# Optimization experiments

Hardware: AMD Instinct MI355X
Metric: run time of the kernel (lower is better)

The kernel has to match this reference:

```python
import jax, jax.numpy as jnp
import numpy as np

B, N, PREV, PRED, H = 16, 64, 6, 30, 256
E = N * (N - 1)
BN_EPS = 1e-5


def _mlp(x, W1, b1, W2, b2, gamma, beta):
    # Two-layer ELU MLP with batch norm over flattened (batch*rows) dim.
    h = jax.nn.elu(x @ W1 + b1)
    h = jax.nn.elu(h @ W2 + b2)
    b, n, d = h.shape
    f = h.reshape(b * n, d)
    mu = f.mean(axis=0)
    var = f.var(axis=0)
    f = (f - mu) * jax.lax.rsqrt(var + BN_EPS) * gamma + beta
    return f.reshape(b, n, d)


def setup_inputs() -> dict:
    key = jax.random.key(0)
    ks = jax.random.split(key, 8)
    # fully-connected directed graph without self loops
    recv, send = np.where(~np.eye(N, dtype=bool))  # each [E]
    rel_rec = jnp.broadcast_to(jax.nn.one_hot(jnp.asarray(recv), N)[None], (B, E, N)).astype(jnp.float32)
    rel_send = jnp.broadcast_to(jax.nn.one_hot(jnp.asarray(send), N)[None], (B, E, N)).astype(jnp.float32)

    def xavier(k, shape):
        fan_in, fan_out = shape
        std = np.sqrt(2.0 / (fan_in + fan_out))
        return jax.random.normal(k, shape, jnp.float32) * std

    return {
        "prev_actor_centers": jax.random.normal(ks[0], (B, N, PREV, 2), jnp.float32) * 10.0,
        "rel_rec": rel_rec,
        "rel_send": rel_send,
        "W_traj": xavier(ks[1], (PREV * 2, H)),
        "b_traj": jnp.full((H,), 0.1, jnp.float32),
        "n2e_W1": xavier(ks[2], (2 * H, H)),
        "n2e_b1": jnp.full((H,), 0.1, jnp.float32),
        "n2e_W2": xavier(ks[3], (H, H)),
        "n2e_b2": jnp.full((H,), 0.1, jnp.float32),
        "n2e_gamma": jnp.ones((H,), jnp.float32),
        "n2e_beta": jnp.zeros((H,), jnp.float32),
        "e2n_W1": xavier(ks[4], (2 * H, H)),
        "e2n_b1": jnp.full((H,), 0.1, jnp.float32),
        "e2n_W2": xavier(ks[5], (H, H)),
        "e2n_b2": jnp.full((H,), 0.1, jnp.float32),
        "e2n_gamma": jnp.ones((H,), jnp.float32),
        "e2n_beta": jnp.zeros((H,), jnp.float32),
        "W_fuse": xavier(ks[6], (2 * H, H)),
        "b_fuse": jnp.full((H,), 0.1, jnp.float32),
        "W_pred": xavier(ks[7], (H, PRED * 2)),
        "b_pred": jnp.full((PRED * 2,), 0.1, jnp.float32),
    }


def reference(prev_actor_centers, rel_rec, rel_send,
              W_traj, b_traj,
              n2e_W1, n2e_b1, n2e_W2, n2e_b2, n2e_gamma, n2e_beta,
              e2n_W1, e2n_b1, e2n_W2, e2n_b2, e2n_gamma, e2n_beta,
              W_fuse, b_fuse, W_pred, b_pred):
    b, n, prev, _ = prev_actor_centers.shape
    # relative displacements, first step zero
    diffs = prev_actor_centers[:, :, 1:, :] - prev_actor_centers[:, :, :-1, :]
    rel_pos = jnp.concatenate([jnp.zeros((b, n, 1, 2), prev_actor_centers.dtype), diffs], axis=2)
    rel_pos = rel_pos.reshape(b, n, prev * 2)
    x = rel_pos @ W_traj + b_traj  # [b, n, H] node features

    # node2edge: gather via one-hot relation matmuls
    receivers = jnp.einsum('ben,bnh->beh', rel_rec, x)
    senders = jnp.einsum('ben,bnh->beh', rel_send, x)
    edges = jnp.concatenate([receivers, senders], axis=-1)  # [b, E, 2H]
    e = _mlp(edges, n2e_W1, n2e_b1, n2e_W2, n2e_b2, n2e_gamma, n2e_beta)

    # edge2node: degree-normalized scatter via transposed relation matmuls
    deg_rec = rel_rec.sum(axis=1)  # [b, n]
    deg_rec = deg_rec + (deg_rec == 0).astype(deg_rec.dtype)
    incoming = jnp.einsum('ben,beh->bnh', rel_rec, e) / deg_rec[..., None]
    deg_send = rel_send.sum(axis=1)
    deg_send = deg_send + (deg_send == 0).astype(deg_send.dtype)
    outgoing = jnp.einsum('ben,beh->bnh', rel_send, e) / deg_send[..., None]
    nodes = jnp.concatenate([incoming, outgoing], axis=-1)  # [b, n, 2H]
    m = _mlp(nodes, e2n_W1, e2n_b1, e2n_W2, e2n_b2, e2n_gamma, e2n_beta)

    fused = jnp.concatenate([x, m], axis=-1) @ W_fuse + b_fuse  # [b, n, H]
    rel = fused @ W_pred + b_pred  # [b, n, PRED*2]

    current_loc = prev_actor_centers[:, :, -1, :]  # [b, n, 2]
    current_loc = jnp.broadcast_to(current_loc[:, :, None, :], (b, n, PRED, 2)).reshape(b, n, PRED * 2)
    pos = jnp.cumsum(rel.reshape(b, n, PRED, 2), axis=2).reshape(b, n, PRED * 2) + current_loc
    return (rel, pos)
```

## Files before the change

### kernel.cpp

```cpp
#include <hip/hip_runtime.h>
#include <hip/hip_bf16.h>

#define BB 16
#define NN 64
#define PREVN 6
#define PREDN 30
#define HH 256
#define EE 4032
#define EROWS (BB*EE)
#define NROWS (BB*NN)

typedef short short8 __attribute__((ext_vector_type(8)));
typedef float f32x4 __attribute__((ext_vector_type(4)));

enum : int {
  OFF_STATS_E = 0,
  OFF_STATS_M = 1024,
  F32_END     = 264192
};
enum : size_t {
  BO_XB    = 0,
  BO_W1TE  = 262144,
  BO_W2TE  = 393216,
  BO_W1TN  = 458752,
  BO_W2TN  = 589824,
  BO_WFT   = 655360,
  BO_WPT   = 786432,
  BO_NODES = 802816,
  BO_M2    = 1327104,
  BO_E2    = 1589248
};

__device__ __forceinline__ float eluf(float v) { return v > 0.f ? v : expm1f(v); }

__device__ __forceinline__ void gl2lds16(const void* g, void* l) {
  __builtin_amdgcn_global_load_lds(
      (const __attribute__((address_space(1))) void*)g,
      (__attribute__((address_space(3))) void*)l, 16, 0, 0);
}

struct PrepArgs {
  const float *centers, *W_traj, *b_traj;
  const float *n2e_W1, *n2e_W2, *e2n_W1, *e2n_W2, *W_fuse, *W_pred;
  float* stats;
  __hip_bfloat16 *xb, *w1te, *w2te, *w1tn, *w2tn, *wft, *wpt;
};

__global__ __launch_bounds__(256) void k_prep(PrepArgs a) {
  __shared__ float t[64][65];
  const int bid = blockIdx.x, tid = threadIdx.x;
  if (bid < 128) {
    const float* W; __hip_bfloat16* WT; int K, lb;
    if (bid < 32)      { W = a.n2e_W1; WT = a.w1te; K = 512; lb = bid; }
    else if (bid < 48) { W = a.n2e_W2; WT = a.w2te; K = 256; lb = bid - 32; }
    else if (bid < 80) { W = a.e2n_W1; WT = a.w1tn; K = 512; lb = bid - 48; }
    else if (bid < 96) { W = a.e2n_W2; WT = a.w2tn; K = 256; lb = bid - 80; }
    else               { W = a.W_fuse; WT = a.wft;  K = 512; lb = bid - 96; }
    int KB = K / 64;
    int k0 = (lb % KB) * 64, n0 = (lb / KB) * 64;
    int tx = tid & 63, ty = tid >> 6;
    #pragma unroll
    for (int i = 0; i < 16; ++i)
      t[ty + i*4][tx] = W[(size_t)(k0 + ty + i*4) * 256 + n0 + tx];
    __syncthreads();
    #pragma unroll
    for (int i = 0; i < 16; ++i)
      WT[(size_t)(n0 + ty + i*4) * K + k0 + tx] = __float2bfloat16(t[tx][ty + i*4]);
  } else if (bid < 192) {
    int idx = (bid - 128) * 256 + tid;
    int c = idx >> 8, k = idx & 255;
    a.wpt[idx] = __float2bfloat16(c < 60 ? a.W_pred[k * 60 + c] : 0.f);
  } else if (bid < 200) {
    a.stats[(bid - 192) * 256 + tid] = 0.f;
  } else {
    int row = bid - 200, col = tid;
    const float* c = a.centers + row * (PREVN * 2);
    float rp[12];
    #pragma unroll
    for (int t2 = 0; t2 < 5; ++t2) {
      rp[2 + 2*t2] = c[(t2+1)*2 + 0] - c[t2*2 + 0];
      rp[3 + 2*t2] = c[(t2+1)*2 + 1] - c[t2*2 + 1];
    }
    float acc = a.b_traj[col];
    #pragma unroll
    for (int k = 2; k < 12; ++k) acc += rp[k] * a.W_traj[k*HH + col];
    a.xb[row*HH + col] = __float2bfloat16(acc);
  }
}

template<int MODE>
__global__ __launch_bounds__(256, 2) void k_mlp3(
    const __hip_bfloat16* __restrict__ A,
    const __hip_bfloat16* __restrict__ W1T,
    const float* __restrict__ b1,
    const __hip_bfloat16* __restrict__ W2T,
    const float* __restrict__ b2,
    __hip_bfloat16* __restrict__ outp,
    float* __restrict__ stats) {
  constexpr int MT = (MODE == 0) ? 4 : 1;
  constexpr int ROWS = MT * 16;
  __shared__ alignas(16) __hip_bfloat16 Wt[256 * 64];
  __shared__ alignas(16) __hip_bfloat16 At[ROWS * 64];
  __shared__ alignas(16) __hip_bfloat16 h1s[ROWS][264];
  const int tid = threadIdx.x;
  const int w = tid >> 6, lane = tid & 63;
  const int m16 = lane & 15, quad = lane >> 4;
  const int ko = quad * 8;
  const int row0 = blockIdx.x * ROWS;
  const int colw = w * 64;
  const int csub = lane >> 3, jl = lane & 7;
  const int jsrc = jl ^ csub;

  const __hip_bfloat16 *ar0[2], *ar1[2];
  #pragma unroll
  for (int t = 0; t < 2; ++t) {
    int i = w + 4 * t;
    if (i < MT * 2) {
      int r = i * 8 + csub;
      int g = row0 + r;
      if (MODE == 0) {
        int b = g / EE; int e = g - b * EE;
        int rc = e / 63; int jj = e - rc * 63;
        int sd = jj + (jj >= rc ? 1 : 0);
        ar0[t] = A + (size_t)(b * NN + rc) * HH;
        ar1[t] = A + (size_t)(b * NN + sd) * HH;
      } else {
        ar0[t] = A + (size_t)g * 512;
        ar1[t] = ar0[t] + 256;
      }
    }
  }
  const int swz0 = ((quad)     ^ (m16 & 7)) * 16;
  const int swz1 = ((quad + 4) ^ (m16 & 7)) * 16;

  f32x4 acc[MT][4];
  #pragma unroll
  for (int jt = 0; jt < 4; ++jt) {
    float bv = b1[colw + jt*16 + m16];
    #pragma unroll
    for (int mt = 0; mt < MT; ++mt) acc[mt][jt] = (f32x4){bv, bv, bv, bv};
  }
  for (int kt = 0; kt < 8; ++kt) {
    const int k0 = kt * 64;
    #pragma unroll
    for (int i = 0; i < 8; ++i) {
      const __hip_bfloat16* gp = W1T + (size_t)(colw + i*8 + csub) * 512 + k0 + jsrc*8;
      gl2lds16(gp, (char*)Wt + w*8192 + i*1024);
    }
    #pragma unroll
    for (int t = 0; t < 2; ++t) {
      int i = w + 4*t;
      if (i < MT*2) {
        const __hip_bfloat16* gp =
            (k0 < 256 ? ar0[t] + k0 : ar1[t] + (k0 - 256)) + jsrc*8;
        gl2lds16(gp, (char*)At + i*1024);
      }
    }
    __syncthreads();
    #pragma unroll
    for (int ks = 0; ks < 2; ++ks) {
      const int sw = ks ? swz1 : swz0;
      short8 af[MT], bf[4];
      #pragma unroll
      for (int mt = 0; mt < MT; ++mt)
        af[mt] = *(const short8*)((const char*)At + (mt*16 + m16)*128 + sw);
      #pragma unroll
      for (int jt = 0; jt < 4; ++jt)
        bf[jt] = *(const short8*)((const char*)Wt + (colw + jt*16 + m16)*128 + sw);
      #pragma unroll
      for (int mt = 0; mt < MT; ++mt)
        #pragma unroll
        for (int jt = 0; jt < 4; ++jt)
          acc[mt][jt] = __builtin_amdgcn_mfma_f32_16x16x32_bf16(af[mt], bf[jt],
                                                                acc[mt][jt], 0, 0, 0);
    }
    __syncthreads();
  }
  #pragma unroll
  for (int mt = 0; mt < MT; ++mt)
    #pragma unroll
    for (int jt = 0; jt < 4; ++jt)
      #pragma unroll
      for (int r = 0; r < 4; ++r)
        h1s[mt*16 + quad*4 + r][colw + jt*16 + m16] =
            __float2bfloat16(eluf(acc[mt][jt][r]));
  __syncthreads();

  f32x4 acc2[MT][4];
  #pragma unroll
  for (int jt = 0; jt < 4; ++jt) {
    float bv = b2[colw + jt*16 + m16];
    #pragma unroll
    for (int mt = 0; mt < MT; ++mt) acc2[mt][jt] = (f32x4){bv, bv, bv, bv};
  }
  for (int kt = 0; kt < 4; ++kt) {
    const int k0 = kt * 64;
    #pragma unroll
    for (int i = 0; i < 8; ++i) {
      const __hip_bfloat16* gp = W2T + (size_t)(colw + i*8 + csub) * 256 + k0 + jsrc*8;
      gl2lds16(gp, (char*)Wt + w*8192 + i*1024);
    }
    __syncthreads();
    #pragma unroll
    for (int ks = 0; ks < 2; ++ks) {
      const int sw = ks ? swz1 : swz0;
      short8 af[MT], bf[4];
      #pragma unroll
      for (int mt = 0; mt < MT; ++mt)
        af[mt] = *(const short8*)((const char*)h1s +
                     (size_t)(mt*16 + m16)*528 + (k0 + ks*32 + ko)*2);
      #pragma unroll
      for (int jt = 0; jt < 4; ++jt)
        bf[jt] = *(const short8*)((const char*)Wt + (colw + jt*16 + m16)*128 + sw);
      #pragma unroll
      for (int mt = 0; mt < MT; ++mt)
        #pragma unroll
        for (int jt = 0; jt < 4; ++jt)
          acc2[mt][jt] = __builtin_amdgcn_mfma_f32_16x16x32_bf16(af[mt], bf[jt],
                                                                 acc2[mt][jt], 0, 0, 0);
    }
    __syncthreads();
  }
  #pragma unroll
  for (int mt = 0; mt < MT; ++mt)
    #pragma unroll
    for (int jt = 0; jt < 4; ++jt)
      #pragma unroll
      for (int r = 0; r < 4; ++r)
        h1s[mt*16 + quad*4 + r][colw + jt*16 + m16] =
            __float2bfloat16(eluf(acc2[mt][jt][r]));
  __syncthreads();

  {
    float s = 0.f, q = 0.f;
    #pragma unroll 8
    for (int r = 0; r < ROWS; ++r) {
      float v = __bfloat162float(h1s[r][tid]);
      s += v; q += v * v;
    }
    atomicAdd(&stats[tid], s);
    atomicAdd(&stats[256 + tid], q);
  }
  #pragma unroll
  for (int i = 0; i < ROWS/8; ++i) {
    int u = i*256 + tid;
    int r = u >> 5, c = (u & 31) * 8;
    *reinterpret_cast<uint4*>(outp + (size_t)(row0 + r)*HH + c) =
        *reinterpret_cast<const uint4*>(&h1s[r][c]);
  }
}

__global__ __launch_bounds__(256) void k_agg2(const __hip_bfloat16* __restrict__ e2,
                                              const float* __restrict__ st,
                                              const float* __restrict__ gam,
                                              const float* __restrict__ bet,
                                              __hip_bfloat16* __restrict__ nodes) {
  __shared__ float red[8][256];
  const int blk = blockIdx.x;
  const int bn = blk >> 1, half = blk & 1;
  const int b = bn >> 6, n = bn & 63;
  const int tid = threadIdx.x;
  const int c8 = (tid & 31) * 8;
  const int rg = tid >> 5;
  const __hip_bfloat16* base = e2 + (size_t)b * EE * HH;
  float s[8] = {0.f,0.f,0.f,0.f,0.f,0.f,0.f,0.f};
  for (int j = rg; j < 63; j += 8) {
    const __hip_bfloat16* rp;
    if (half == 0) {
      rp = base + (size_t)(n*63 + j)*HH;
    } else {
      int i = j + (j >= n ? 1 : 0);
      int e = i*63 + n - (n > i ? 1 : 0);
      rp = base + (size_t)e*HH;
    }
    union { uint4 u; __hip_bfloat16 h[8]; } v;
    v.u = *reinterpret_cast<const uint4*>(rp + c8);
    #pragma unroll
    for (int jj = 0; jj < 8; ++jj) s[jj] += __bfloat162float(v.h[jj]);
  }
  #pragma unroll
  for (int jj = 0; jj < 8; jj += 4)
    *reinterpret_cast<float4*>(&red[rg][c8 + jj]) =
        (float4){s[jj], s[jj+1], s[jj+2], s[jj+3]};
  __syncthreads();
  float S = 0.f;
  #pragma unroll
  for (int r = 0; r < 8; ++r) S += red[r][tid];
  const float inv = 1.f / (float)EROWS;
  float mean = st[tid] * inv;
  float var  = fmaxf(st[256 + tid] * inv - mean*mean, 0.f);
  float a = gam[tid] * rsqrtf(var + 1e-5f);
  float c0 = bet[tid] - mean * a;
  nodes[(size_t)bn*512 + half*256 + tid] = __float2bfloat16(a * S * (1.f/63.f) + c0);
}

__global__ __launch_bounds__(256) void k_head2(
    const __hip_bfloat16* __restrict__ xb,
    const __hip_bfloat16* __restrict__ m2,
    const float* __restrict__ stM,
    const float* __restrict__ gam,
    const float* __restrict__ bet,
    const __hip_bfloat16* __restrict__ WfT,
    const float* __restrict__ bfv,
    const __hip_bfloat16* __restrict__ WpT,
    const float* __restrict__ bp,
    const float* __restrict__ centers,
    float* __restrict__ out) {
  __shared__ alignas(16) __hip_bfloat16 hs[16][264];
  __shared__ float rl[16][64];
  __shared__ float bnA[256], bnC[256];
  const int tid = threadIdx.x;
  const int w = tid >> 6, lane = tid & 63;
  const int m16 = lane & 15, quad = lane >> 4;
  const int ko = quad * 8;
  const int row0 = blockIdx.x * 16;
  const int colw = w * 64;

  {
    const float inv = 1.f / (float)NROWS;
    float mean = stM[tid] * inv;
    float var  = fmaxf(stM[256 + tid] * inv - mean*mean, 0.f);
    float am = gam[tid] * rsqrtf(var + 1e-5f);
    bnA[tid] = am;
    bnC[tid] = bet[tid] - mean * am;
  }
  __syncthreads();

  f32x4 acc[4];
  #pragma unroll
  for (int jt = 0; jt < 4; ++jt) {
    float bv = bfv[colw + jt*16 + m16];
    acc[jt] = (f32x4){bv, bv, bv, bv};
  }
  #pragma unroll
  for (int ks = 0; ks < 16; ++ks) {
    short8 af;
    if (ks < 8) {
      af = *reinterpret_cast<const short8*>(
          xb + (size_t)(row0 + m16)*256 + ks*32 + ko);
    } else {
      int k0 = (ks - 8)*32 + ko;
      union { uint4 u; __hip_bfloat16 h[8]; } v;
      v.u = *reinterpret_cast<const uint4*>(m2 + (size_t)(row0 + m16)*256 + k0);
      union { short8 s8; __hip_bfloat16 h[8]; } o;
      #pragma unroll
      for (int j = 0; j < 8; ++j)
        o.h[j] = __float2bfloat16(bnA[k0+j] * __bfloat162float(v.h[j]) + bnC[k0+j]);
      af = o.s8;
    }
    short8 bf[4];
    #pragma unroll
    for (int jt = 0; jt < 4; ++jt)
      bf[jt] = *reinterpret_cast<const short8*>(
          WfT + (size_t)(colw + jt*16 + m16)*512 + ks*32 + ko);
    #pragma unroll
    for (int jt = 0; jt < 4; ++jt)
      acc[jt] = __builtin_amdgcn_mfma_f32_16x16x32_bf16(af, bf[jt], acc[jt], 0, 0, 0);
  }
  #pragma unroll
  for (int jt = 0; jt < 4; ++jt)
    #pragma unroll
    for (int r = 0; r < 4; ++r)
      hs[quad*4 + r][colw + jt*16 + m16] = __float2bfloat16(acc[jt][r]);
  __syncthreads();

  if (w == 0) {
    f32x4 acc2[4];
    #pragma unroll
    for (int jt = 0; jt < 4; ++jt) {
      int c = jt*16 + m16;
      float bv = (c < 60) ? bp[c] : 0.f;
      acc2[jt] = (f32x4){bv, bv, bv, bv};
    }
    #pragma unroll
    for (int ks = 0; ks < 8; ++ks) {
      short8 af = *reinterpret_cast<const short8*>(&hs[m16][ks*32 + ko]);
      short8 bf[4];
      #pragma unroll
      for (int jt = 0; jt < 4; ++jt)
        bf[jt] = *reinterpret_cast<const short8*>(
            WpT + (size_t)(jt*16 + m16)*256 + ks*32 + ko);
      #pragma unroll
      for (int jt = 0; jt < 4; ++jt)
        acc2[jt] = __builtin_amdgcn_mfma_f32_16x16x32_bf16(af, bf[jt], acc2[jt], 0, 0, 0);
    }
    #pragma unroll
    for (int jt = 0; jt < 4; ++jt) {
      int c = jt*16 + m16;
      #pragma unroll
      for (int r = 0; r < 4; ++r) {
        int lr = quad*4 + r;
        rl[lr][c] = acc2[jt][r];
        if (c < 60) out[(size_t)(row0 + lr)*60 + c] = acc2[jt][r];
      }
    }
  }
  __syncthreads();

  if (tid < 32) {
    int lr = tid >> 1, xy = tid & 1;
    int grow = row0 + lr;
    float run = centers[(size_t)(grow*PREVN + 5)*2 + xy];
    #pragma unroll
    for (int p = 0; p < PREDN; ++p) {
      run += rl[lr][2*p + xy];
      out[61440 + (size_t)grow*60 + 2*p + xy] = run;
    }
  }
}

extern "C" void kernel_launch(void* const* d_in, const int* in_sizes, int n_in,
                              void* d_out, int out_size, void* d_ws, size_t ws_size,
                              hipStream_t stream) {
  const float* centers = (const float*)d_in[0];
  float* ws = (float*)d_ws;
  __hip_bfloat16* wb = (__hip_bfloat16*)(ws + F32_END);

  PrepArgs pa;
  pa.centers = centers;
  pa.W_traj = (const float*)d_in[3];  pa.b_traj = (const float*)d_in[4];
  pa.n2e_W1 = (const float*)d_in[5];  pa.n2e_W2 = (const float*)d_in[7];
  pa.e2n_W1 = (const float*)d_in[11]; pa.e2n_W2 = (const float*)d_in[13];
  pa.W_fuse = (const float*)d_in[17]; pa.W_pred = (const float*)d_in[19];
  pa.stats = ws;
  pa.xb = wb + BO_XB; pa.w1te = wb + BO_W1TE; pa.w2te = wb + BO_W2TE;
  pa.w1tn = wb + BO_W1TN; pa.w2tn = wb + BO_W2TN; pa.wft = wb + BO_WFT;
  pa.wpt = wb + BO_WPT;

  const float* n2e_b1 = (const float*)d_in[6];
  const float* n2e_b2 = (const float*)d_in[8];
  const float* n2e_g  = (const float*)d_in[9];
  const float* n2e_be = (const float*)d_in[10];
  const float* e2n_b1 = (const float*)d_in[12];
  const float* e2n_b2 = (const float*)d_in[14];
  const float* e2n_g  = (const float*)d_in[15];
  const float* e2n_be = (const float*)d_in[16];
  const float* b_fuse = (const float*)d_in[18];
  const float* b_pred = (const float*)d_in[20];

  k_prep<<<1224, 256, 0, stream>>>(pa);
  k_mlp3<0><<<EROWS/64, 256, 0, stream>>>(wb + BO_XB, wb + BO_W1TE, n2e_b1,
                                          wb + BO_W2TE, n2e_b2,
                                          wb + BO_E2, ws + OFF_STATS_E);
  k_agg2<<<2*NROWS, 256, 0, stream>>>(wb + BO_E2, ws + OFF_STATS_E, n2e_g, n2e_be,
                                      wb + BO_NODES);
  k_mlp3<1><<<NROWS/16, 256, 0, stream>>>(wb + BO_NODES, wb + BO_W1TN, e2n_b1,
                                          wb + BO_W2TN, e2n_b2,
                                          wb + BO_M2, ws + OFF_STATS_M);
  k_head2<<<NROWS/16, 256, 0, stream>>>(wb + BO_XB, wb + BO_M2, ws + OFF_STATS_M,
                                        e2n_g, e2n_be, wb + BO_WFT, b_fuse,
                                        wb + BO_WPT, b_pred, centers,
                                        (float*)d_out);
}
```

Baseline: 215.2 us.

## Double-buffer weight tiles in LDS and load A fragments directly to registers

The fused two-layer MLP kernel now double-buffers the weight K-tiles in LDS. Each tile is prefetched asynchronously with global_load_lds while the MFMAs work on the current tile, and explicit vmcnt waits replace the per-iteration __syncthreads. The A operand, including the gathered receiver/sender rows, is read straight from global memory into register double buffers instead of being staged through LDS. This relies on each wave touching only its own weight slice, and the launch bound drops to one block per CU because the larger LDS footprint lowers occupancy.

```diff
diff --git a/kernel.cpp b/kernel.cpp
--- a/kernel.cpp
+++ b/kernel.cpp
@@ -39,6 +39,10 @@
       (__attribute__((address_space(3))) void*)l, 16, 0, 0);
 }
 
+template<int N> __device__ __forceinline__ void waitvm() {
+  asm volatile("s_waitcnt vmcnt(%0)" :: "n"(N) : "memory");
+}
+
 struct PrepArgs {
   const float *centers, *W_traj, *b_traj;
   const float *n2e_W1, *n2e_W2, *e2n_W1, *e2n_W2, *W_fuse, *W_pred;
@@ -89,7 +93,7 @@
 }
 
 template<int MODE>
-__global__ __launch_bounds__(256, 2) void k_mlp3(
+__global__ __launch_bounds__(256, 1) void k_mlp5(
     const __hip_bfloat16* __restrict__ A,
     const __hip_bfloat16* __restrict__ W1T,
     const float* __restrict__ b1,
@@ -99,8 +103,8 @@
     float* __restrict__ stats) {
   constexpr int MT = (MODE == 0) ? 4 : 1;
   constexpr int ROWS = MT * 16;
-  __shared__ alignas(16) __hip_bfloat16 Wt[256 * 64];
-  __shared__ alignas(16) __hip_bfloat16 At[ROWS * 64];
+  constexpr int AL = MT * 2;
+  __shared__ alignas(16) __hip_bfloat16 Wd[2][256 * 64];
   __shared__ alignas(16) __hip_bfloat16 h1s[ROWS][264];
   const int tid = threadIdx.x;
   const int w = tid >> 6, lane = tid & 63;
@@ -110,29 +114,44 @@
   const int colw = w * 64;
   const int csub = lane >> 3, jl = lane & 7;
   const int jsrc = jl ^ csub;
-
-  const __hip_bfloat16 *ar0[2], *ar1[2];
-  #pragma unroll
-  for (int t = 0; t < 2; ++t) {
-    int i = w + 4 * t;
-    if (i < MT * 2) {
-      int r = i * 8 + csub;
-      int g = row0 + r;
-      if (MODE == 0) {
-        int b = g / EE; int e = g - b * EE;
-        int rc = e / 63; int jj = e - rc * 63;
-        int sd = jj + (jj >= rc ? 1 : 0);
-        ar0[t] = A + (size_t)(b * NN + rc) * HH;
-        ar1[t] = A + (size_t)(b * NN + sd) * HH;
-      } else {
-        ar0[t] = A + (size_t)g * 512;
-        ar1[t] = ar0[t] + 256;
-      }
-    }
-  }
   const int swz0 = ((quad)     ^ (m16 & 7)) * 16;
   const int swz1 = ((quad + 4) ^ (m16 & 7)) * 16;
 
+  const char* abase = (const char*)A;
+  int off0[MT], off1[MT];
+  #pragma unroll
+  for (int mt = 0; mt < MT; ++mt) {
+    int g = row0 + mt*16 + m16;
+    if (MODE == 0) {
+      int b = g / EE; int e = g - b*EE;
+      int rc = e / 63; int jj = e - rc*63;
+      int sd = jj + (jj >= rc ? 1 : 0);
+      off0[mt] = (b*NN + rc) * 512;
+      off1[mt] = (b*NN + sd) * 512;
+    } else {
+      off0[mt] = g * 1024;
+      off1[mt] = off0[mt] + 512;
+    }
+  }
+
+  auto stageW = [&](const __hip_bfloat16* WT, int Kst, int k0, int buf) {
+    #pragma unroll
+    for (int i = 0; i < 8; ++i) {
+      const __hip_bfloat16* gp = WT + (size_t)(colw + i*8 + csub)*Kst + k0 + jsrc*8;
+      gl2lds16(gp, (char*)&Wd[buf][0] + w*8192 + i*1024);
+    }
+  };
+  auto loadA = [&](int kt, short8* dst) {
+    #pragma unroll
+    for (int mt = 0; mt < MT; ++mt)
+      #pragma unroll
+      for (int ks = 0; ks < 2; ++ks) {
+        int koff = (kt < 4 ? kt : kt - 4)*128 + ks*64 + ko*2;
+        int ob = (kt < 4 ? off0[mt] : off1[mt]);
+        dst[mt*2 + ks] = *(const short8*)(abase + ob + koff);
+      }
+  };
+
   f32x4 acc[MT][4];
   #pragma unroll
   for (int jt = 0; jt < 4; ++jt) {
@@ -140,78 +159,66 @@
     #pragma unroll
     for (int mt = 0; mt < MT; ++mt) acc[mt][jt] = (f32x4){bv, bv, bv, bv};
   }
+  short8 aA[AL], aB[AL];
+  stageW(W1T, 512, 0, 0);
+  loadA(0, aA);
+  #pragma unroll
   for (int kt = 0; kt < 8; ++kt) {
-    const int k0 = kt * 64;
-    #pragma unroll
-    for (int i = 0; i < 8; ++i) {
-      const __hip_bfloat16* gp = W1T + (size_t)(colw + i*8 + csub) * 512 + k0 + jsrc*8;
-      gl2lds16(gp, (char*)Wt + w*8192 + i*1024);
-    }
-    #pragma unroll
-    for (int t = 0; t < 2; ++t) {
-      int i = w + 4*t;
-      if (i < MT*2) {
-        const __hip_bfloat16* gp =
-            (k0 < 256 ? ar0[t] + k0 : ar1[t] + (k0 - 256)) + jsrc*8;
-        gl2lds16(gp, (char*)At + i*1024);
-      }
-    }
-    __syncthreads();
+    short8* aCur = (kt & 1) ? aB : aA;
+    short8* aNxt = (kt & 1) ? aA : aB;
+    if (kt < 7) stageW(W1T, 512, (kt+1)*64, (kt+1) & 1);
+    if (kt < 7) waitvm<8 + AL>(); else waitvm<AL>();
+    if (kt < 7) loadA(kt+1, aNxt);
+    const int cb = kt & 1;
+    #pragma unroll
+    for (int ks = 0; ks < 2; ++ks) {
+      const int sw = ks ? swz1 : swz0;
+      short8 bf[4];
+      #pragma unroll
+      for (int jt = 0; jt < 4; ++jt)
+        bf[jt] = *(const short8*)((const char*)&Wd[cb][0] + (colw + jt*16 + m16)*128 + sw);
+      #pragma unroll
+      for (int mt = 0; mt < MT; ++mt)
+        #pragma unroll
+        for (int jt = 0; jt < 4; ++jt)
+          acc[mt][jt] = __builtin_amdgcn_mfma_f32_16x16x32_bf16(aCur[mt*2+ks], bf[jt],
+                                                                acc[mt][jt], 0, 0, 0);
+    }
+  }
+  #pragma unroll
+  for (int mt = 0; mt < MT; ++mt)
+    #pragma unroll
+    for (int jt = 0; jt < 4; ++jt)
+      #pragma unroll
+      for (int r = 0; r < 4; ++r)
+        h1s[mt*16 + quad*4 + r][colw + jt*16 + m16] =
+            __float2bfloat16(eluf(acc[mt][jt][r]));
+  __syncthreads();
+
+  f32x4 acc2[MT][4];
+  #pragma unroll
+  for (int jt = 0; jt < 4; ++jt) {
+    float bv = b2[colw + jt*16 + m16];
+    #pragma unroll
+    for (int mt = 0; mt < MT; ++mt) acc2[mt][jt] = (f32x4){bv, bv, bv, bv};
+  }
+  stageW(W2T, 256, 0, 0);
+  #pragma unroll
+  for (int kt = 0; kt < 4; ++kt) {
+    if (kt < 3) stageW(W2T, 256, (kt+1)*64, (kt+1) & 1);
+    if (kt < 3) waitvm<8>(); else waitvm<0>();
+    const int cb = kt & 1;
     #pragma unroll
     for (int ks = 0; ks < 2; ++ks) {
       const int sw = ks ? swz1 : swz0;
       short8 af[MT], bf[4];
       #pragma unroll
       for (int mt = 0; mt < MT; ++mt)
-        af[mt] = *(const short8*)((const char*)At + (mt*16 + m16)*128 + sw);
+        af[mt] = *(const short8*)((const char*)h1s +
+                     (size_t)(mt*16 + m16)*528 + (kt*64 + ks*32 + ko)*2);
       #pragma unroll
       for (int jt = 0; jt < 4; ++jt)
-        bf[jt] = *(const short8*)((const char*)Wt + (colw + jt*16 + m16)*128 + sw);
-      #pragma unroll
-      for (int mt = 0; mt < MT; ++mt)
-        #pragma unroll
-        for (int jt = 0; jt < 4; ++jt)
-          acc[mt][jt] = __builtin_amdgcn_mfma_f32_16x16x32_bf16(af[mt], bf[jt],
-                                                                acc[mt][jt], 0, 0, 0);
-    }
-    __syncthreads();
-  }
-  #pragma unroll
-  for (int mt = 0; mt < MT; ++mt)
-    #pragma unroll
-    for (int jt = 0; jt < 4; ++jt)
-      #pragma unroll
-      for (int r = 0; r < 4; ++r)
-        h1s[mt*16 + quad*4 + r][colw + jt*16 + m16] =
-            __float2bfloat16(eluf(acc[mt][jt][r]));
-  __syncthreads();
-
-  f32x4 acc2[MT][4];
-  #pragma unroll
-  for (int jt = 0; jt < 4; ++jt) {
-    float bv = b2[colw + jt*16 + m16];
-    #pragma unroll
-    for (int mt = 0; mt < MT; ++mt) acc2[mt][jt] = (f32x4){bv, bv, bv, bv};
-  }
-  for (int kt = 0; kt < 4; ++kt) {
-    const int k0 = kt * 64;
-    #pragma unroll
-    for (int i = 0; i < 8; ++i) {
-      const __hip_bfloat16* gp = W2T + (size_t)(colw + i*8 + csub) * 256 + k0 + jsrc*8;
-      gl2lds16(gp, (char*)Wt + w*8192 + i*1024);
-    }
-    __syncthreads();
-    #pragma unroll
-    for (int ks = 0; ks < 2; ++ks) {
-      const int sw = ks ? swz1 : swz0;
-      short8 af[MT], bf[4];
-      #pragma unroll
-      for (int mt = 0; mt < MT; ++mt)
-        af[mt] = *(const short8*)((const char*)h1s +
-                     (size_t)(mt*16 + m16)*528 + (k0 + ks*32 + ko)*2);
-      #pragma unroll
-      for (int jt = 0; jt < 4; ++jt)
-        bf[jt] = *(const short8*)((const char*)Wt + (colw + jt*16 + m16)*128 + sw);
+        bf[jt] = *(const short8*)((const char*)&Wd[cb][0] + (colw + jt*16 + m16)*128 + sw);
       #pragma unroll
       for (int mt = 0; mt < MT; ++mt)
         #pragma unroll
@@ -219,8 +226,8 @@
           acc2[mt][jt] = __builtin_amdgcn_mfma_f32_16x16x32_bf16(af[mt], bf[jt],
                                                                  acc2[mt][jt], 0, 0, 0);
     }
-    __syncthreads();
-  }
+  }
+  __syncthreads();
   #pragma unroll
   for (int mt = 0; mt < MT; ++mt)
     #pragma unroll
@@ -439,12 +446,12 @@
   const float* b_pred = (const float*)d_in[20];
 
   k_prep<<<1224, 256, 0, stream>>>(pa);
-  k_mlp3<0><<<EROWS/64, 256, 0, stream>>>(wb + BO_XB, wb + BO_W1TE, n2e_b1,
+  k_mlp5<0><<<EROWS/64, 256, 0, stream>>>(wb + BO_XB, wb + BO_W1TE, n2e_b1,
                                           wb + BO_W2TE, n2e_b2,
                                           wb + BO_E2, ws + OFF_STATS_E);
   k_agg2<<<2*NROWS, 256, 0, stream>>>(wb + BO_E2, ws + OFF_STATS_E, n2e_g, n2e_be,
                                       wb + BO_NODES);
-  k_mlp3<1><<<NROWS/16, 256, 0, stream>>>(wb + BO_NODES, wb + BO_W1TN, e2n_b1,
+  k_mlp5<1><<<NROWS/16, 256, 0, stream>>>(wb + BO_NODES, wb + BO_W1TN, e2n_b1,
                                           wb + BO_W2TN, e2n_b2,
                                           wb + BO_M2, ws + OFF_STATS_M);
   k_head2<<<NROWS/16, 256, 0, stream>>>(wb + BO_XB, wb + BO_M2, ws + OFF_STATS_M,
```

Result: slower. 248.5 us (+15.5%).

## Factor first edge-MLP layer into per-node receiver and sender projections

Applied to the files above, without the earlier changes.

The first n2e layer is linear in the concatenated receiver/sender features, so it is computed once per node as two 256x256 projections (k_xrs) and then summed per edge before ELU. The edge kernel no longer runs the K=512 GEMM over 64K edge rows; it gathers the precomputed node projections from LDS and only runs the second layer. This cuts the first-layer FLOPs by roughly the node degree. The cost is an extra launch and rounding the intermediate projections to bf16 before the add.

```diff
diff --git a/kernel.cpp b/kernel.cpp
--- a/kernel.cpp
+++ b/kernel.cpp
@@ -16,6 +16,7 @@
 enum : int {
   OFF_STATS_E = 0,
   OFF_STATS_M = 1024,
+  OFF_XRS     = 2048,
   F32_END     = 264192
 };
 enum : size_t {
@@ -88,8 +89,174 @@
   }
 }
 
-template<int MODE>
-__global__ __launch_bounds__(256, 2) void k_mlp3(
+__global__ __launch_bounds__(256) void k_xrs(
+    const __hip_bfloat16* __restrict__ xb,
+    const __hip_bfloat16* __restrict__ W1T,
+    const float* __restrict__ b1,
+    __hip_bfloat16* __restrict__ xrs) {
+  const int tid = threadIdx.x;
+  const int w = tid >> 6, lane = tid & 63;
+  const int m16 = lane & 15, quad = lane >> 4;
+  const int ko = quad * 8;
+  const int half = blockIdx.x >> 4;
+  const int row0 = (blockIdx.x & 15) * 64;
+  const int colw = w * 64;
+  __hip_bfloat16* dst = xrs + (size_t)half * 262144;
+
+  f32x4 acc[4][4];
+  #pragma unroll
+  for (int jt = 0; jt < 4; ++jt) {
+    float bv = half ? 0.f : b1[colw + jt*16 + m16];
+    #pragma unroll
+    for (int mt = 0; mt < 4; ++mt) acc[mt][jt] = (f32x4){bv, bv, bv, bv};
+  }
+  #pragma unroll
+  for (int ks = 0; ks < 8; ++ks) {
+    short8 af[4], bf[4];
+    #pragma unroll
+    for (int mt = 0; mt < 4; ++mt)
+      af[mt] = *reinterpret_cast<const short8*>(
+          xb + (size_t)(row0 + mt*16 + m16)*256 + ks*32 + ko);
+    #pragma unroll
+    for (int jt = 0; jt < 4; ++jt)
+      bf[jt] = *reinterpret_cast<const short8*>(
+          W1T + (size_t)(colw + jt*16 + m16)*512 + half*256 + ks*32 + ko);
+    #pragma unroll
+    for (int mt = 0; mt < 4; ++mt)
+      #pragma unroll
+      for (int jt = 0; jt < 4; ++jt)
+        acc[mt][jt] = __builtin_amdgcn_mfma_f32_16x16x32_bf16(af[mt], bf[jt],
+                                                              acc[mt][jt], 0, 0, 0);
+  }
+  #pragma unroll
+  for (int mt = 0; mt < 4; ++mt)
+    #pragma unroll
+    for (int jt = 0; jt < 4; ++jt)
+      #pragma unroll
+      for (int r = 0; r < 4; ++r)
+        dst[(size_t)(row0 + mt*16 + quad*4 + r)*256 + colw + jt*16 + m16] =
+            __float2bfloat16(acc[mt][jt][r]);
+}
+
+__global__ __launch_bounds__(256, 2) void k_mlp6(
+    const __hip_bfloat16* __restrict__ xrs,
+    const __hip_bfloat16* __restrict__ W2T,
+    const float* __restrict__ b2,
+    __hip_bfloat16* __restrict__ outp,
+    float* __restrict__ stats) {
+  __shared__ alignas(16) char reg1[33792];
+  __shared__ alignas(16) __hip_bfloat16 h1s[64][264];
+  const int tid = threadIdx.x;
+  const int w = tid >> 6, lane = tid & 63;
+  const int m16 = lane & 15, quad = lane >> 4;
+  const int ko = quad * 8;
+  const int blk = blockIdx.x;
+  const int bb = blk / 63, lb = blk - bb*63;
+  const int row0 = blk * 64;
+  const int n0 = (lb * 64) / 63;
+  const int colw = w * 64;
+  const int csub = lane >> 3, jl = lane & 7;
+  const int jsrc = jl ^ csub;
+  const int swz0 = ((quad)     ^ (m16 & 7)) * 16;
+  const int swz1 = ((quad + 4) ^ (m16 & 7)) * 16;
+
+  const char* xsb = (const char*)(xrs + 262144 + (size_t)bb*64*256);
+  #pragma unroll
+  for (int i = 0; i < 8; ++i) {
+    int seg = w*8 + i;
+    gl2lds16(xsb + seg*1024 + lane*16, reg1 + seg*1024);
+  }
+  if (w == 0)
+    gl2lds16((const char*)(xrs + (size_t)(bb*64 + n0)*256) + lane*16, reg1 + 32768);
+  __syncthreads();
+
+  {
+    const int ty = tid >> 7;
+    const int c2 = (tid & 127) * 2;
+    #pragma unroll 4
+    for (int r2 = 0; r2 < 32; ++r2) {
+      int r = ty*32 + r2;
+      int e = lb*64 + r;
+      int rc = e / 63; int jj = e - rc*63;
+      int sd = jj + (jj >= rc ? 1 : 0);
+      __hip_bfloat162 xa = *reinterpret_cast<const __hip_bfloat162*>(
+          reg1 + 32768 + (rc - n0)*512 + c2*2);
+      __hip_bfloat162 xs2 = *reinterpret_cast<const __hip_bfloat162*>(
+          reg1 + sd*512 + c2*2);
+      __hip_bfloat162 o;
+      o.x = __float2bfloat16(eluf(__bfloat162float(xa.x) + __bfloat162float(xs2.x)));
+      o.y = __float2bfloat16(eluf(__bfloat162float(xa.y) + __bfloat162float(xs2.y)));
+      *reinterpret_cast<__hip_bfloat162*>(&h1s[r][c2]) = o;
+    }
+  }
+  __syncthreads();
+
+  __hip_bfloat16* Wt = (__hip_bfloat16*)reg1;
+  f32x4 acc2[4][4];
+  #pragma unroll
+  for (int jt = 0; jt < 4; ++jt) {
+    float bv = b2[colw + jt*16 + m16];
+    #pragma unroll
+    for (int mt = 0; mt < 4; ++mt) acc2[mt][jt] = (f32x4){bv, bv, bv, bv};
+  }
+  for (int kt = 0; kt < 4; ++kt) {
+    const int k0 = kt * 64;
+    #pragma unroll
+    for (int i = 0; i < 8; ++i) {
+      const __hip_bfloat16* gp = W2T + (size_t)(colw + i*8 + csub) * 256 + k0 + jsrc*8;
+      gl2lds16(gp, (char*)Wt + w*8192 + i*1024);
+    }
+    __syncthreads();
+    #pragma unroll
+    for (int ks = 0; ks < 2; ++ks) {
+      const int sw = ks ? swz1 : swz0;
+      short8 af[4], bf[4];
+      #pragma unroll
+      for (int mt = 0; mt < 4; ++mt)
+        af[mt] = *(const short8*)((const char*)h1s +
+                     (size_t)(mt*16 + m16)*528 + (k0 + ks*32 + ko)*2);
+      #pragma unroll
+      for (int jt = 0; jt < 4; ++jt)
+        bf[jt] = *(const short8*)((const char*)Wt + (colw + jt*16 + m16)*128 + sw);
+      #pragma unroll
+      for (int mt = 0; mt < 4; ++mt)
+        #pragma unroll
+        for (int jt = 0; jt < 4; ++jt)
+          acc2[mt][jt] = __builtin_amdgcn_mfma_f32_16x16x32_bf16(af[mt], bf[jt],
+                                                                 acc2[mt][jt], 0, 0, 0);
+    }
+    __syncthreads();
+  }
+  #pragma unroll
+  for (int mt = 0; mt < 4; ++mt)
+    #pragma unroll
+    for (int jt = 0; jt < 4; ++jt)
+      #pragma unroll
+      for (int r = 0; r < 4; ++r)
+        h1s[mt*16 + quad*4 + r][colw + jt*16 + m16] =
+            __float2bfloat16(eluf(acc2[mt][jt][r]));
+  __syncthreads();
+
+  {
+    float s = 0.f, q = 0.f;
+    #pragma unroll 8
+    for (int r = 0; r < 64; ++r) {
+      float v = __bfloat162float(h1s[r][tid]);
+      s += v; q += v * v;
+    }
+    atomicAdd(&stats[tid], s);
+    atomicAdd(&stats[256 + tid], q);
+  }
+  #pragma unroll
+  for (int i = 0; i < 8; ++i) {
+    int u = i*256 + tid;
+    int r = u >> 5, c = (u & 31) * 8;
+    *reinterpret_cast<uint4*>(outp + (size_t)(row0 + r)*HH + c) =
+        *reinterpret_cast<const uint4*>(&h1s[r][c]);
+  }
+}
+
+__global__ __launch_bounds__(256, 2) void k_mlp3n(
     const __hip_bfloat16* __restrict__ A,
     const __hip_bfloat16* __restrict__ W1T,
     const float* __restrict__ b1,
@@ -97,48 +264,32 @@
     const float* __restrict__ b2,
     __hip_bfloat16* __restrict__ outp,
     float* __restrict__ stats) {
-  constexpr int MT = (MODE == 0) ? 4 : 1;
-  constexpr int ROWS = MT * 16;
   __shared__ alignas(16) __hip_bfloat16 Wt[256 * 64];
-  __shared__ alignas(16) __hip_bfloat16 At[ROWS * 64];
-  __shared__ alignas(16) __hip_bfloat16 h1s[ROWS][264];
+  __shared__ alignas(16) __hip_bfloat16 At[16 * 64];
+  __shared__ alignas(16) __hip_bfloat16 h1s[16][264];
   const int tid = threadIdx.x;
   const int w = tid >> 6, lane = tid & 63;
   const int m16 = lane & 15, quad = lane >> 4;
   const int ko = quad * 8;
-  const int row0 = blockIdx.x * ROWS;
+  const int row0 = blockIdx.x * 16;
   const int colw = w * 64;
   const int csub = lane >> 3, jl = lane & 7;
   const int jsrc = jl ^ csub;
-
-  const __hip_bfloat16 *ar0[2], *ar1[2];
-  #pragma unroll
-  for (int t = 0; t < 2; ++t) {
-    int i = w + 4 * t;
-    if (i < MT * 2) {
-      int r = i * 8 + csub;
-      int g = row0 + r;
-      if (MODE == 0) {
-        int b = g / EE; int e = g - b * EE;
-        int rc = e / 63; int jj = e - rc * 63;
-        int sd = jj + (jj >= rc ? 1 : 0);
-        ar0[t] = A + (size_t)(b * NN + rc) * HH;
-        ar1[t] = A + (size_t)(b * NN + sd) * HH;
-      } else {
-        ar0[t] = A + (size_t)g * 512;
-        ar1[t] = ar0[t] + 256;
-      }
-    }
-  }
   const int swz0 = ((quad)     ^ (m16 & 7)) * 16;
   const int swz1 = ((quad + 4) ^ (m16 & 7)) * 16;
 
-  f32x4 acc[MT][4];
+  const __hip_bfloat16 *ar0 = nullptr, *ar1 = nullptr;
+  if (w < 2) {
+    int r = w * 8 + csub;
+    ar0 = A + (size_t)(row0 + r) * 512;
+    ar1 = ar0 + 256;
+  }
+
+  f32x4 acc[4];
   #pragma unroll
   for (int jt = 0; jt < 4; ++jt) {
     float bv = b1[colw + jt*16 + m16];
-    #pragma unroll
-    for (int mt = 0; mt < MT; ++mt) acc[mt][jt] = (f32x4){bv, bv, bv, bv};
+    acc[jt] = (f32x4){bv, bv, bv, bv};
   }
   for (int kt = 0; kt < 8; ++kt) {
     const int k0 = kt * 64;
@@ -147,51 +298,37 @@
       const __hip_bfloat16* gp = W1T + (size_t)(colw + i*8 + csub) * 512 + k0 + jsrc*8;
       gl2lds16(gp, (char*)Wt + w*8192 + i*1024);
     }
-    #pragma unroll
-    for (int t = 0; t < 2; ++t) {
-      int i = w + 4*t;
-      if (i < MT*2) {
-        const __hip_bfloat16* gp =
-            (k0 < 256 ? ar0[t] + k0 : ar1[t] + (k0 - 256)) + jsrc*8;
-        gl2lds16(gp, (char*)At + i*1024);
-      }
+    if (w < 2) {
+      const __hip_bfloat16* gp = (k0 < 256 ? ar0 + k0 : ar1 + (k0 - 256)) + jsrc*8;
+      gl2lds16(gp, (char*)At + w*1024);
     }
     __syncthreads();
     #pragma unroll
     for (int ks = 0; ks < 2; ++ks) {
       const int sw = ks ? swz1 : swz0;
-      short8 af[MT], bf[4];
-      #pragma unroll
-      for (int mt = 0; mt < MT; ++mt)
-        af[mt] = *(const short8*)((const char*)At + (mt*16 + m16)*128 + sw);
+      short8 af = *(const short8*)((const char*)At + m16*128 + sw);
+      short8 bf[4];
       #pragma unroll
       for (int jt = 0; jt < 4; ++jt)
         bf[jt] = *(const short8*)((const char*)Wt + (colw + jt*16 + m16)*128 + sw);
       #pragma unroll
-      for (int mt = 0; mt < MT; ++mt)
-        #pragma unroll
-        for (int jt = 0; jt < 4; ++jt)
-          acc[mt][jt] = __builtin_amdgcn_mfma_f32_16x16x32_bf16(af[mt], bf[jt],
-                                                                acc[mt][jt], 0, 0, 0);
-    }
-    __syncthreads();
-  }
-  #pragma unroll
-  for (int mt = 0; mt < MT; ++mt)
-    #pragma unroll
-    for (int jt = 0; jt < 4; ++jt)
-      #pragma unroll
-      for (int r = 0; r < 4; ++r)
-        h1s[mt*16 + quad*4 + r][colw + jt*16 + m16] =
-            __float2bfloat16(eluf(acc[mt][jt][r]));
-  __syncthreads();
-
-  f32x4 acc2[MT][4];
+      for (int jt = 0; jt < 4; ++jt)
+        acc[jt] = __builtin_amdgcn_mfma_f32_16x16x32_bf16(af, bf[jt], acc[jt], 0, 0, 0);
+    }
+    __syncthreads();
+  }
+  #pragma unroll
+  for (int jt = 0; jt < 4; ++jt)
+    #pragma unroll
+    for (int r = 0; r < 4; ++r)
+      h1s[quad*4 + r][colw + jt*16 + m16] = __float2bfloat16(eluf(acc[jt][r]));
+  __syncthreads();
+
+  f32x4 acc2[4];
   #pragma unroll
   for (int jt = 0; jt < 4; ++jt) {
     float bv = b2[colw + jt*16 + m16];
-    #pragma unroll
-    for (int mt = 0; mt < MT; ++mt) acc2[mt][jt] = (f32x4){bv, bv, bv, bv};
+    acc2[jt] = (f32x4){bv, bv, bv, bv};
   }
   for (int kt = 0; kt < 4; ++kt) {
     const int k0 = kt * 64;
@@ -204,37 +341,29 @@
     #pragma unroll
     for (int ks = 0; ks < 2; ++ks) {
       const int sw = ks ? swz1 : swz0;
-      short8 af[MT], bf[4];
-      #pragma unroll
-      for (int mt = 0; mt < MT; ++mt)
-        af[mt] = *(const short8*)((const char*)h1s +
-                     (size_t)(mt*16 + m16)*528 + (k0 + ks*32 + ko)*2);
+      short8 af = *(const short8*)((const char*)h1s +
+                     (size_t)m16*528 + (k0 + ks*32 + ko)*2);
+      short8 bf[4];
       #pragma unroll
       for (int jt = 0; jt < 4; ++jt)
         bf[jt] = *(const short8*)((const char*)Wt + (colw + jt*16 + m16)*128 + sw);
       #pragma unroll
-      for (int mt = 0; mt < MT; ++mt)
-        #pragma unroll
-        for (int jt = 0; jt < 4; ++jt)
-          acc2[mt][jt] = __builtin_amdgcn_mfma_f32_16x16x32_bf16(af[mt], bf[jt],
-                                                                 acc2[mt][jt], 0, 0, 0);
-    }
-    __syncthreads();
-  }
-  #pragma unroll
-  for (int mt = 0; mt < MT; ++mt)
-    #pragma unroll
-    for (int jt = 0; jt < 4; ++jt)
-      #pragma unroll
-      for (int r = 0; r < 4; ++r)
-        h1s[mt*16 + quad*4 + r][colw + jt*16 + m16] =
-            __float2bfloat16(eluf(acc2[mt][jt][r]));
+      for (int jt = 0; jt < 4; ++jt)
+        acc2[jt] = __builtin_amdgcn_mfma_f32_16x16x32_bf16(af, bf[jt], acc2[jt], 0, 0, 0);
+    }
+    __syncthreads();
+  }
+  #pragma unroll
+  for (int jt = 0; jt < 4; ++jt)
+    #pragma unroll
+    for (int r = 0; r < 4; ++r)
+      h1s[quad*4 + r][colw + jt*16 + m16] = __float2bfloat16(eluf(acc2[jt][r]));
   __syncthreads();
 
   {
     float s = 0.f, q = 0.f;
     #pragma unroll 8
-    for (int r = 0; r < ROWS; ++r) {
+    for (int r = 0; r < 16; ++r) {
       float v = __bfloat162float(h1s[r][tid]);
       s += v; q += v * v;
     }
@@ -242,7 +371,7 @@
     atomicAdd(&stats[256 + tid], q);
   }
   #pragma unroll
-  for (int i = 0; i < ROWS/8; ++i) {
+  for (int i = 0; i < 2; ++i) {
     int u = i*256 + tid;
     int r = u >> 5, c = (u & 31) * 8;
     *reinterpret_cast<uint4*>(outp + (size_t)(row0 + r)*HH + c) =
@@ -415,6 +544,7 @@
   const float* centers = (const float*)d_in[0];
   float* ws = (float*)d_ws;
   __hip_bfloat16* wb = (__hip_bfloat16*)(ws + F32_END);
+  __hip_bfloat16* xrs = (__hip_bfloat16*)(ws + OFF_XRS);
 
   PrepArgs pa;
   pa.centers = centers;
@@ -439,14 +569,14 @@
   const float* b_pred = (const float*)d_in[20];
 
   k_prep<<<1224, 256, 0, stream>>>(pa);
-  k_mlp3<0><<<EROWS/64, 256, 0, stream>>>(wb + BO_XB, wb + BO_W1TE, n2e_b1,
-                                          wb + BO_W2TE, n2e_b2,
-                                          wb + BO_E2, ws + OFF_STATS_E);
+  k_xrs<<<32, 256, 0, stream>>>(wb + BO_XB, wb + BO_W1TE, n2e_b1, xrs);
+  k_mlp6<<<EROWS/64, 256, 0, stream>>>(xrs, wb + BO_W2TE, n2e_b2,
+                                       wb + BO_E2, ws + OFF_STATS_E);
   k_agg2<<<2*NROWS, 256, 0, stream>>>(wb + BO_E2, ws + OFF_STATS_E, n2e_g, n2e_be,
                                       wb + BO_NODES);
-  k_mlp3<1><<<NROWS/16, 256, 0, stream>>>(wb + BO_NODES, wb + BO_W1TN, e2n_b1,
-                                          wb + BO_W2TN, e2n_b2,
-                                          wb + BO_M2, ws + OFF_STATS_M);
+  k_mlp3n<<<NROWS/16, 256, 0, stream>>>(wb + BO_NODES, wb + BO_W1TN, e2n_b1,
+                                        wb + BO_W2TN, e2n_b2,
+                                        wb + BO_M2, ws + OFF_STATS_M);
   k_head2<<<NROWS/16, 256, 0, stream>>>(wb + BO_XB, wb + BO_M2, ws + OFF_STATS_M,
                                         e2n_g, e2n_be, wb + BO_WFT, b_fuse,
                                         wb + BO_WPT, b_pred, centers,
```

After: 210.7 us. 2.1% less time.
